# Kernel optimization log

Hardware: AMD Instinct MI355X
Metric: run time of the kernel (lower is better)

## Reference

```python
import jax, jax.numpy as jnp
import numpy as np

NUM_HEADS = 8
EMBED = 512
HEAD_DIM = EMBED // NUM_HEADS
B, S = 4, 2048


def setup_inputs() -> dict:
    key = jax.random.key(0)
    ks = jax.random.split(key, 8)
    sc = 0.02
    return {
        "values": jax.random.normal(ks[0], (B, S, EMBED), dtype=jnp.float32),
        "keys": jax.random.normal(ks[1], (B, S, EMBED), dtype=jnp.float32),
        "query": jax.random.normal(ks[2], (B, S, EMBED), dtype=jnp.float32),
        "Wv": jax.random.normal(ks[3], (HEAD_DIM, HEAD_DIM), dtype=jnp.float32) * sc,
        "Wk": jax.random.normal(ks[4], (HEAD_DIM, HEAD_DIM), dtype=jnp.float32) * sc,
        "Wq": jax.random.normal(ks[5], (HEAD_DIM, HEAD_DIM), dtype=jnp.float32) * sc,
        "Wo": jax.random.normal(ks[6], (EMBED, EMBED), dtype=jnp.float32) * sc,
        "bo": jnp.zeros((EMBED,), dtype=jnp.float32),
    }


def reference(values, keys, query, Wv, Wk, Wq, Wo, bo):
    b, s, _ = query.shape
    # split heads: [B, S, H, D]
    v = values.reshape(b, s, NUM_HEADS, HEAD_DIM)
    k = keys.reshape(b, s, NUM_HEADS, HEAD_DIM)
    q = query.reshape(b, s, NUM_HEADS, HEAD_DIM)
    # per-head linear (nn.Linear: x @ W.T), weights shared across heads
    v = jnp.einsum("bshd,ed->bshe", v, Wv)
    k = jnp.einsum("bshd,ed->bshe", k, Wk)
    q = jnp.einsum("bshd,ed->bshe", q, Wq)
    # energy: [B, H, Q, K]
    energy = jnp.einsum("bqhd,bkhd->bhqk", q, k)
    # NOTE: original scales by sqrt(embed_size), not sqrt(head_dim)
    attn = jax.nn.softmax(energy / jnp.sqrt(jnp.float32(EMBED)), axis=-1)
    out = jnp.einsum("bhqk,bkhd->bqhd", attn, v).reshape(b, s, EMBED)
    return out @ Wo.T + bo
```

## Files before the change

### kernel.cpp

```cpp
#include <hip/hip_runtime.h>

#define H 8
#define D 64
#define E 512
#define BATCH 4
#define SEQ 2048

typedef __bf16 bf16v8 __attribute__((ext_vector_type(8)));
typedef float f32v4 __attribute__((ext_vector_type(4)));
typedef unsigned int u32v4 __attribute__((ext_vector_type(4)));
typedef unsigned short u16v4 __attribute__((ext_vector_type(4)));

#define MFMA16(a,b,c) __builtin_amdgcn_mfma_f32_16x16x32_bf16(a,b,c,0,0,0)

#define AS1 __attribute__((address_space(1)))
#define AS3 __attribute__((address_space(3)))
#define GLDS16(g, l) __builtin_amdgcn_global_load_lds((const AS1 void*)(g), (AS3 void*)(l), 16, 0, 0)

static __device__ __forceinline__ unsigned short f2bf(float f) {
  unsigned u = __builtin_bit_cast(unsigned, f);
  u += 0x7fffu + ((u >> 16) & 1u);
  return (unsigned short)(u >> 16);
}

static __device__ __forceinline__ bf16v8 lds16(const char* p) {
  return __builtin_bit_cast(bf16v8, *(const u32v4*)p);
}

__global__ void prep_w(const float* __restrict__ Wo, const float* __restrict__ Wv,
                       const float* __restrict__ Wq, const float* __restrict__ Wk,
                       unsigned short* __restrict__ Wo2, unsigned short* __restrict__ MT) {
  int bx = blockIdx.x;
  if (bx < 1024) {
    int i = bx * 256 + threadIdx.x;
    int n = i >> 9, c = i & 511;
    int h = c >> 6, d = c & 63;
    float acc = 0.f;
    for (int e = 0; e < 64; ++e) acc += Wo[n*512 + h*64 + e] * Wv[e*64 + d];
    Wo2[n*512 + c] = f2bf(acc);
  } else {
    int i = (bx - 1024) * 256 + threadIdx.x;
    int d2 = i >> 6, d1 = i & 63;
    float acc = 0.f;
    for (int e = 0; e < 64; ++e) acc += Wq[e*64 + d1] * Wk[e*64 + d2];
    MT[d2*64 + d1] = f2bf(acc * 0.04419417382415922f);
  }
}

__global__ void prep_tok(const float* __restrict__ v, const float* __restrict__ keys,
                         unsigned short* __restrict__ vT, unsigned short* __restrict__ kb) {
  __shared__ float tile[64][65];
  int bh = blockIdx.y;
  int b = bh >> 3, h = bh & 7;
  int sc = blockIdx.x;
  int t = threadIdx.x;
  int flat = bh * 32 + sc;
  {
    const float* kp = keys + (size_t)flat * 4096;
    unsigned short* ko = kb + (size_t)flat * 4096;
    #pragma unroll
    for (int i = 0; i < 4; ++i) {
      f32v4 x = *(const f32v4*)(kp + (i*256 + t)*4);
      u16v4 o = { f2bf(x[0]), f2bf(x[1]), f2bf(x[2]), f2bf(x[3]) };
      *(u16v4*)(ko + (i*256 + t)*4) = o;
    }
  }
  #pragma unroll
  for (int i = 0; i < 16; ++i) {
    int idx = i*256 + t; int si = idx >> 6, d = idx & 63;
    tile[si][d] = v[((size_t)(b*SEQ + sc*64 + si))*E + h*64 + d];
  }
  __syncthreads();
  #pragma unroll
  for (int i = 0; i < 16; ++i) {
    int idx = i*256 + t; int d = idx >> 6, si = idx & 63;
    vT[((size_t)(bh*64 + d))*SEQ + sc*64 + si] = f2bf(tile[si][d]);
  }
}

__global__ __launch_bounds__(256) void proj_qm(const float* __restrict__ q,
                                               const unsigned short* __restrict__ MT,
                                               unsigned short* __restrict__ qm) {
  __shared__ __align__(16) char lds[16384 + 8192];
  char* xl = lds;
  char* ml = lds + 16384;
  int h = blockIdx.y;
  int t0 = blockIdx.x * 128;
  int tid = threadIdx.x;
  #pragma unroll
  for (int i = 0; i < 8; ++i) {
    int c = i*256 + tid;
    int row = c >> 4, cc = c & 15;
    f32v4 xv = *(const f32v4*)(q + (size_t)(t0 + row)*E + h*64 + cc*4);
    u16v4 o = { f2bf(xv[0]), f2bf(xv[1]), f2bf(xv[2]), f2bf(xv[3]) };
    int off = row*128 + ((((cc >> 1) ^ (row & 7))) << 4) + (cc & 1)*8;
    *(u16v4*)(xl + off) = o;
  }
  #pragma unroll
  for (int i = 0; i < 2; ++i) {
    int c = i*256 + tid; int row = c >> 3, cc = c & 7;
    *(u32v4*)(ml + row*128 + ((cc ^ (row & 7)) << 4)) = *(const u32v4*)(MT + row*64 + cc*8);
  }
  __syncthreads();
  int w = tid >> 6, lane = tid & 63, hi = lane >> 4, lo = lane & 15;
  f32v4 acc[2][4] = {};
  bf16v8 a[2][2], bfr[4][2];
  #pragma unroll
  for (int mt = 0; mt < 2; ++mt)
    #pragma unroll
    for (int kk = 0; kk < 2; ++kk) {
      int row = w*32 + mt*16 + lo;
      a[mt][kk] = lds16(xl + row*128 + (((kk*4 + hi) ^ (row & 7)) << 4));
    }
  #pragma unroll
  for (int nt = 0; nt < 4; ++nt)
    #pragma unroll
    for (int kk = 0; kk < 2; ++kk) {
      int row = nt*16 + lo;
      bfr[nt][kk] = lds16(ml + row*128 + (((kk*4 + hi) ^ (row & 7)) << 4));
    }
  #pragma unroll
  for (int mt = 0; mt < 2; ++mt)
    #pragma unroll
    for (int nt = 0; nt < 4; ++nt)
      #pragma unroll
      for (int kk = 0; kk < 2; ++kk)
        acc[mt][nt] = MFMA16(a[mt][kk], bfr[nt][kk], acc[mt][nt]);
  #pragma unroll
  for (int mt = 0; mt < 2; ++mt)
    #pragma unroll
    for (int nt = 0; nt < 4; ++nt)
      #pragma unroll
      for (int r = 0; r < 4; ++r) {
        int tok = t0 + w*32 + mt*16 + 4*hi + r;
        qm[(size_t)tok*E + h*64 + nt*16 + lo] = f2bf(acc[mt][nt][r]);
      }
}

__global__ __launch_bounds__(256, 4) void attn(const unsigned short* __restrict__ qm,
                                               const unsigned short* __restrict__ kb,
                                               const unsigned short* __restrict__ vT,
                                               unsigned short* __restrict__ ao) {
  __shared__ __align__(16) char lds[40960];
  int bh = blockIdx.y, b = bh >> 3, h = bh & 7;
  int qt = blockIdx.x;
  int tid = threadIdx.x, w = tid >> 6, lane = tid & 63, hi = lane >> 4, lo = lane & 15;
  char* pw = lds + 32768 + w*2048;

  const unsigned short* kbase = kb + (size_t)(b*SEQ)*E + h*64;
  const unsigned short* vbase = vT + (size_t)bh*64*SEQ;

  int srow = tid >> 3, scc = tid & 7;

  bf16v8 qa[2];
  {
    int qrow = qt*64 + w*16 + lo;
    const unsigned short* qp = qm + ((size_t)(b*SEQ + qrow))*E + h*64;
    qa[0] = __builtin_bit_cast(bf16v8, *(const u32v4*)(qp + hi*8));
    qa[1] = __builtin_bit_cast(bf16v8, *(const u32v4*)(qp + 32 + hi*8));
  }
  f32v4 oacc[4] = {};
  float lsum[4] = {0.f, 0.f, 0.f, 0.f};

  #pragma unroll
  for (int i = 0; i < 2; ++i) {
    int row = i*32 + srow;
    int sc = scc ^ (row & 7);
    GLDS16(kbase + (size_t)row*E + sc*8,   lds        + i*4096 + w*1024);
    GLDS16(vbase + (size_t)row*SEQ + sc*8, lds + 8192 + i*4096 + w*1024);
  }
  __syncthreads();

  for (int kt = 0; kt < 32; ++kt) {
    const char* klc = lds + (kt & 1)*16384;
    const char* vlc = klc + 8192;
    if (kt < 31) {
      char* kln = lds + ((kt & 1) ^ 1)*16384;
      char* vln = kln + 8192;
      #pragma unroll
      for (int i = 0; i < 2; ++i) {
        int row = i*32 + srow;
        int sc = scc ^ (row & 7);
        GLDS16(kbase + (size_t)((kt+1)*64 + row)*E + sc*8, kln + i*4096 + w*1024);
        GLDS16(vbase + (size_t)row*SEQ + (kt+1)*64 + sc*8, vln + i*4096 + w*1024);
      }
    }
    f32v4 sacc[4] = {};
    #pragma unroll
    for (int nt = 0; nt < 4; ++nt)
      #pragma unroll
      for (int kk = 0; kk < 2; ++kk) {
        int row = nt*16 + lo;
        bf16v8 kf = lds16(klc + row*128 + (((kk*4 + hi) ^ (row & 7)) << 4));
        sacc[nt] = MFMA16(qa[kk], kf, sacc[nt]);
      }
    #pragma unroll
    for (int nt = 0; nt < 4; ++nt)
      #pragma unroll
      for (int r = 0; r < 4; ++r) {
        float p = exp2f(sacc[nt][r] * 1.4426950408889634f);
        lsum[r] += p;
        int qrw = 4*hi + r;
        *(unsigned short*)(pw + qrw*128 + ((nt*32 + lo*2) ^ ((qrw & 7) << 4))) = f2bf(p);
      }
    asm volatile("s_waitcnt lgkmcnt(0)" ::: "memory");
    __builtin_amdgcn_sched_barrier(0);
    #pragma unroll
    for (int ks = 0; ks < 2; ++ks) {
      bf16v8 pa = lds16(pw + lo*128 + (((ks*4 + hi) ^ (lo & 7)) << 4));
      #pragma unroll
      for (int dt = 0; dt < 4; ++dt) {
        int row = dt*16 + lo;
        bf16v8 vf = lds16(vlc + row*128 + (((ks*4 + hi) ^ (row & 7)) << 4));
        oacc[dt] = MFMA16(pa, vf, oacc[dt]);
      }
    }
    __syncthreads();
  }
  #pragma unroll
  for (int r = 0; r < 4; ++r) {
    #pragma unroll
    for (int m = 1; m < 16; m <<= 1) lsum[r] += __shfl_xor(lsum[r], m, 64);
    lsum[r] = __builtin_amdgcn_rcpf(lsum[r]);
  }
  #pragma unroll
  for (int dt = 0; dt < 4; ++dt)
    #pragma unroll
    for (int r = 0; r < 4; ++r) {
      int tok = b*SEQ + qt*64 + w*16 + 4*hi + r;
      ao[(size_t)tok*E + h*64 + dt*16 + lo] = f2bf(oacc[dt][r] * lsum[r]);
    }
}

__global__ __launch_bounds__(256, 4) void final_gemm(const unsigned short* __restrict__ ao,
                                                     const unsigned short* __restrict__ wo2,
                                                     const float* __restrict__ bo,
                                                     float* __restrict__ out) {
  __shared__ __align__(16) char lds[32768];
  int m0 = blockIdx.x * 64, n0 = blockIdx.y * 64;
  int tid = threadIdx.x, w = tid >> 6, lane = tid & 63, hi = lane >> 4, lo = lane & 15;
  int wm = (w >> 1) * 32, wn = (w & 1) * 32;
  int srow = tid >> 3, scc = tid & 7;
  f32v4 acc[2][2] = {};
  #pragma unroll
  for (int i = 0; i < 2; ++i) {
    int row = i*32 + srow;
    int sc = scc ^ (row & 7);
    GLDS16(ao  + (size_t)(m0 + row)*E + sc*8, lds        + i*4096 + w*1024);
    GLDS16(wo2 + (size_t)(n0 + row)*E + sc*8, lds + 8192 + i*4096 + w*1024);
  }
  __syncthreads();
  for (int kt = 0; kt < 8; ++kt) {
    const char* al = lds + (kt & 1)*16384;
    const char* bl = al + 8192;
    if (kt < 7) {
      char* an = lds + ((kt & 1) ^ 1)*16384;
      char* bn = an + 8192;
      #pragma unroll
      for (int i = 0; i < 2; ++i) {
        int row = i*32 + srow;
        int sc = scc ^ (row & 7);
        GLDS16(ao  + (size_t)(m0 + row)*E + (kt+1)*64 + sc*8, an + i*4096 + w*1024);
        GLDS16(wo2 + (size_t)(n0 + row)*E + (kt+1)*64 + sc*8, bn + i*4096 + w*1024);
      }
    }
    #pragma unroll
    for (int kk = 0; kk < 2; ++kk) {
      bf16v8 af[2], bfv[2];
      #pragma unroll
      for (int mt = 0; mt < 2; ++mt) {
        int row = wm + mt*16 + lo;
        af[mt] = lds16(al + row*128 + (((kk*4 + hi) ^ (row & 7)) << 4));
      }
      #pragma unroll
      for (int nt = 0; nt < 2; ++nt) {
        int row = wn + nt*16 + lo;
        bfv[nt] = lds16(bl + row*128 + (((kk*4 + hi) ^ (row & 7)) << 4));
      }
      #pragma unroll
      for (int mt = 0; mt < 2; ++mt)
        #pragma unroll
        for (int nt = 0; nt < 2; ++nt)
          acc[mt][nt] = MFMA16(af[mt], bfv[nt], acc[mt][nt]);
    }
    __syncthreads();
  }
  #pragma unroll
  for (int nt = 0; nt < 2; ++nt) {
    float bias = bo[n0 + wn + nt*16 + lo];
    #pragma unroll
    for (int mt = 0; mt < 2; ++mt)
      #pragma unroll
      for (int r = 0; r < 4; ++r)
        out[(size_t)(m0 + wm + mt*16 + 4*hi + r)*E + n0 + wn + nt*16 + lo] =
            acc[mt][nt][r] + bias;
  }
}

extern "C" void kernel_launch(void* const* d_in, const int* in_sizes, int n_in,
                              void* d_out, int out_size, void* d_ws, size_t ws_size,
                              hipStream_t stream) {
  const float* values = (const float*)d_in[0];
  const float* keys   = (const float*)d_in[1];
  const float* query  = (const float*)d_in[2];
  const float* Wv     = (const float*)d_in[3];
  const float* Wk     = (const float*)d_in[4];
  const float* Wq     = (const float*)d_in[5];
  const float* Wo     = (const float*)d_in[6];
  const float* bo     = (const float*)d_in[7];
  float* out = (float*)d_out;
  char* ws = (char*)d_ws;

  unsigned short* MT  = (unsigned short*)(ws);
  unsigned short* Wo2 = (unsigned short*)(ws + 8192);
  unsigned short* kb  = (unsigned short*)(ws + (1u  << 20));
  unsigned short* vT  = (unsigned short*)(ws + (9u  << 20));
  unsigned short* qmp = (unsigned short*)(ws + (17u << 20));
  unsigned short* ao  = (unsigned short*)(ws + (25u << 20));

  prep_w    <<<1040, 256, 0, stream>>>(Wo, Wv, Wq, Wk, Wo2, MT);
  prep_tok  <<<dim3(32, 32), 256, 0, stream>>>(values, keys, vT, kb);
  proj_qm   <<<dim3(64, 8),  256, 0, stream>>>(query, MT, qmp);
  attn      <<<dim3(32, 32), 256, 0, stream>>>(qmp, kb, vT, ao);
  final_gemm<<<dim3(128, 8), 256, 0, stream>>>(ao, Wo2, bo, out);
}
```

Measured before the change: 191.4 us.

## Fuse query projection into attention kernel and use hardware exp2

Removes the separate proj_qm kernel and computes each block's projected query tile inside the attention kernel prologue. The fp32 query is converted to bf16 into spare LDS, multiplied by MT with MFMA, and staged through the per-wave P buffer to form the A fragments. This saves one launch and the round trip of the bf16 qm buffer through global memory. The softmax exp now uses the raw hardware exp2 builtin, which skips the library's range handling.

Measured after the change: 178.2 us. 1.07x faster.

```diff
diff --git a/kernel.cpp b/kernel.cpp
--- a/kernel.cpp
+++ b/kernel.cpp
@@ -21,6 +21,14 @@
   unsigned u = __builtin_bit_cast(unsigned, f);
   u += 0x7fffu + ((u >> 16) & 1u);
   return (unsigned short)(u >> 16);
+}
+
+static __device__ __forceinline__ float exp2_hw(float x) {
+#if __has_builtin(__builtin_amdgcn_exp2f)
+  return __builtin_amdgcn_exp2f(x);
+#else
+  return exp2f(x);
+#endif
 }
 
 static __device__ __forceinline__ bf16v8 lds16(const char* p) {
@@ -78,66 +86,8 @@
   }
 }
 
-__global__ __launch_bounds__(256) void proj_qm(const float* __restrict__ q,
+__global__ __launch_bounds__(256, 4) void attn(const float* __restrict__ query,
                                                const unsigned short* __restrict__ MT,
-                                               unsigned short* __restrict__ qm) {
-  __shared__ __align__(16) char lds[16384 + 8192];
-  char* xl = lds;
-  char* ml = lds + 16384;
-  int h = blockIdx.y;
-  int t0 = blockIdx.x * 128;
-  int tid = threadIdx.x;
-  #pragma unroll
-  for (int i = 0; i < 8; ++i) {
-    int c = i*256 + tid;
-    int row = c >> 4, cc = c & 15;
-    f32v4 xv = *(const f32v4*)(q + (size_t)(t0 + row)*E + h*64 + cc*4);
-    u16v4 o = { f2bf(xv[0]), f2bf(xv[1]), f2bf(xv[2]), f2bf(xv[3]) };
-    int off = row*128 + ((((cc >> 1) ^ (row & 7))) << 4) + (cc & 1)*8;
-    *(u16v4*)(xl + off) = o;
-  }
-  #pragma unroll
-  for (int i = 0; i < 2; ++i) {
-    int c = i*256 + tid; int row = c >> 3, cc = c & 7;
-    *(u32v4*)(ml + row*128 + ((cc ^ (row & 7)) << 4)) = *(const u32v4*)(MT + row*64 + cc*8);
-  }
-  __syncthreads();
-  int w = tid >> 6, lane = tid & 63, hi = lane >> 4, lo = lane & 15;
-  f32v4 acc[2][4] = {};
-  bf16v8 a[2][2], bfr[4][2];
-  #pragma unroll
-  for (int mt = 0; mt < 2; ++mt)
-    #pragma unroll
-    for (int kk = 0; kk < 2; ++kk) {
-      int row = w*32 + mt*16 + lo;
-      a[mt][kk] = lds16(xl + row*128 + (((kk*4 + hi) ^ (row & 7)) << 4));
-    }
-  #pragma unroll
-  for (int nt = 0; nt < 4; ++nt)
-    #pragma unroll
-    for (int kk = 0; kk < 2; ++kk) {
-      int row = nt*16 + lo;
-      bfr[nt][kk] = lds16(ml + row*128 + (((kk*4 + hi) ^ (row & 7)) << 4));
-    }
-  #pragma unroll
-  for (int mt = 0; mt < 2; ++mt)
-    #pragma unroll
-    for (int nt = 0; nt < 4; ++nt)
-      #pragma unroll
-      for (int kk = 0; kk < 2; ++kk)
-        acc[mt][nt] = MFMA16(a[mt][kk], bfr[nt][kk], acc[mt][nt]);
-  #pragma unroll
-  for (int mt = 0; mt < 2; ++mt)
-    #pragma unroll
-    for (int nt = 0; nt < 4; ++nt)
-      #pragma unroll
-      for (int r = 0; r < 4; ++r) {
-        int tok = t0 + w*32 + mt*16 + 4*hi + r;
-        qm[(size_t)tok*E + h*64 + nt*16 + lo] = f2bf(acc[mt][nt][r]);
-      }
-}
-
-__global__ __launch_bounds__(256, 4) void attn(const unsigned short* __restrict__ qm,
                                                const unsigned short* __restrict__ kb,
                                                const unsigned short* __restrict__ vT,
                                                unsigned short* __restrict__ ao) {
@@ -152,16 +102,6 @@
 
   int srow = tid >> 3, scc = tid & 7;
 
-  bf16v8 qa[2];
-  {
-    int qrow = qt*64 + w*16 + lo;
-    const unsigned short* qp = qm + ((size_t)(b*SEQ + qrow))*E + h*64;
-    qa[0] = __builtin_bit_cast(bf16v8, *(const u32v4*)(qp + hi*8));
-    qa[1] = __builtin_bit_cast(bf16v8, *(const u32v4*)(qp + 32 + hi*8));
-  }
-  f32v4 oacc[4] = {};
-  float lsum[4] = {0.f, 0.f, 0.f, 0.f};
-
   #pragma unroll
   for (int i = 0; i < 2; ++i) {
     int row = i*32 + srow;
@@ -169,7 +109,58 @@
     GLDS16(kbase + (size_t)row*E + sc*8,   lds        + i*4096 + w*1024);
     GLDS16(vbase + (size_t)row*SEQ + sc*8, lds + 8192 + i*4096 + w*1024);
   }
+  {
+    char* xl = lds + 16384;
+    char* ml = lds + 24576;
+    #pragma unroll
+    for (int i = 0; i < 4; ++i) {
+      int c = i*256 + tid;
+      int row = c >> 4, cc = c & 15;
+      f32v4 xv = *(const f32v4*)(query + (size_t)(b*SEQ + qt*64 + row)*E + h*64 + cc*4);
+      u16v4 o = { f2bf(xv[0]), f2bf(xv[1]), f2bf(xv[2]), f2bf(xv[3]) };
+      int off = row*128 + ((((cc >> 1) ^ (row & 7))) << 4) + (cc & 1)*8;
+      *(u16v4*)(xl + off) = o;
+    }
+    #pragma unroll
+    for (int i = 0; i < 2; ++i) {
+      int c = i*256 + tid; int row = c >> 3, cc = c & 7;
+      *(u32v4*)(ml + row*128 + ((cc ^ (row & 7)) << 4)) = *(const u32v4*)(MT + row*64 + cc*8);
+    }
+  }
   __syncthreads();
+
+  bf16v8 qa[2];
+  {
+    char* xl = lds + 16384;
+    char* ml = lds + 24576;
+    f32v4 acc[4] = {};
+    #pragma unroll
+    for (int kk = 0; kk < 2; ++kk) {
+      int arow = w*16 + lo;
+      bf16v8 af = lds16(xl + arow*128 + (((kk*4 + hi) ^ (arow & 7)) << 4));
+      #pragma unroll
+      for (int nt = 0; nt < 4; ++nt) {
+        int brow = nt*16 + lo;
+        bf16v8 bf_ = lds16(ml + brow*128 + (((kk*4 + hi) ^ (brow & 7)) << 4));
+        acc[nt] = MFMA16(af, bf_, acc[nt]);
+      }
+    }
+    #pragma unroll
+    for (int nt = 0; nt < 4; ++nt)
+      #pragma unroll
+      for (int r = 0; r < 4; ++r) {
+        int qrw = 4*hi + r;
+        *(unsigned short*)(pw + qrw*128 + ((nt*32 + lo*2) ^ ((qrw & 7) << 4))) = f2bf(acc[nt][r]);
+      }
+    asm volatile("s_waitcnt lgkmcnt(0)" ::: "memory");
+    __builtin_amdgcn_sched_barrier(0);
+    qa[0] = lds16(pw + lo*128 + (((0*4 + hi) ^ (lo & 7)) << 4));
+    qa[1] = lds16(pw + lo*128 + (((1*4 + hi) ^ (lo & 7)) << 4));
+  }
+  __syncthreads();
+
+  f32v4 oacc[4] = {};
+  float lsum[4] = {0.f, 0.f, 0.f, 0.f};
 
   for (int kt = 0; kt < 32; ++kt) {
     const char* klc = lds + (kt & 1)*16384;
@@ -198,7 +189,7 @@
     for (int nt = 0; nt < 4; ++nt)
       #pragma unroll
       for (int r = 0; r < 4; ++r) {
-        float p = exp2f(sacc[nt][r] * 1.4426950408889634f);
+        float p = exp2_hw(sacc[nt][r] * 1.4426950408889634f);
         lsum[r] += p;
         int qrw = 4*hi + r;
         *(unsigned short*)(pw + qrw*128 + ((nt*32 + lo*2) ^ ((qrw & 7) << 4))) = f2bf(p);
@@ -315,12 +306,10 @@
   unsigned short* Wo2 = (unsigned short*)(ws + 8192);
   unsigned short* kb  = (unsigned short*)(ws + (1u  << 20));
   unsigned short* vT  = (unsigned short*)(ws + (9u  << 20));
-  unsigned short* qmp = (unsigned short*)(ws + (17u << 20));
-  unsigned short* ao  = (unsigned short*)(ws + (25u << 20));
+  unsigned short* ao  = (unsigned short*)(ws + (17u << 20));
 
   prep_w    <<<1040, 256, 0, stream>>>(Wo, Wv, Wq, Wk, Wo2, MT);
   prep_tok  <<<dim3(32, 32), 256, 0, stream>>>(values, keys, vT, kb);
-  proj_qm   <<<dim3(64, 8),  256, 0, stream>>>(query, MT, qmp);
-  attn      <<<dim3(32, 32), 256, 0, stream>>>(qmp, kb, vT, ao);
+  attn      <<<dim3(32, 32), 256, 0, stream>>>(query, MT, kb, vT, ao);
   final_gemm<<<dim3(128, 8), 256, 0, stream>>>(ao, Wo2, bo, out);
 }
```
